# Kernel optimization log

Hardware: AMD Instinct MI355X
Metric: run time of the kernel (lower is better)

Reference implementation:

```python
import jax, jax.numpy as jnp
import numpy as np

BS, N, D = 64, 2048, 512

def setup_inputs() -> dict:
    key = jax.random.key(0)
    ks = jax.random.split(key, 9)
    M = jax.random.uniform(ks[0], (BS, N, D), dtype=jnp.float32)          # memory, uniform(0,1) like M_init
    k = jax.random.normal(ks[1], (BS, D), dtype=jnp.float32)              # key/query
    beta = 5.0 * jax.random.uniform(ks[2], (BS, 1), dtype=jnp.float32)    # content sharpness > 0
    g = jax.random.uniform(ks[3], (BS, 1), dtype=jnp.float32)             # interpolation gate in (0,1)
    s = jax.nn.softmax(jax.random.normal(ks[4], (BS, 3), dtype=jnp.float32), axis=-1)  # shift dist over [-1,0,1]
    y = 1.0 + 2.0 * jax.random.uniform(ks[5], (BS, 1), dtype=jnp.float32) # sharpen exponent >= 1
    e = jax.random.uniform(ks[6], (BS, D), dtype=jnp.float32)             # erase vector in (0,1)
    a = jax.random.normal(ks[7], (BS, D), dtype=jnp.float32)              # add vector
    w_prev = jax.nn.softmax(jax.random.normal(ks[8], (BS, N), dtype=jnp.float32), axis=-1)
    return {"M": M, "k": k, "beta": beta, "g": g, "s": s, "y": y,
            "e": e, "a": a, "w_prev": w_prev}

def reference(M, k, beta, g, s, y, e, a, w_prev):
    # --- content focus: cosine similarity, scaled by beta, softmax over N ---
    dot = jnp.einsum('bnd,bd->bn', M, k)                                   # [bs, N]
    denom = jnp.linalg.norm(M, axis=-1) * jnp.linalg.norm(k, axis=-1, keepdims=True)
    w = jax.nn.softmax((dot / denom) * beta, axis=1)
    # --- location focus: interpolate with previous weights ---
    w = g * w + (1.0 - g) * w_prev
    # --- circular convolution with 3-tap shift kernel s (offsets -1,0,+1) ---
    # original: window [w[i-1], w[i], w[i+1]] dotted with flipped s -> s2*w[i-1]+s1*w[i]+s0*w[i+1]
    w = (s[:, 2:3] * jnp.roll(w, 1, axis=1)
         + s[:, 1:2] * w
         + s[:, 0:1] * jnp.roll(w, -1, axis=1))
    # --- sharpen ---
    wp = w ** y
    w = wp / jnp.sum(wp, axis=1, keepdims=True)                            # [bs, N]
    # --- read ---
    r = jnp.einsum('bn,bnd->bd', w, M)                                     # [bs, D]
    # --- write: M[i] <- M[i] * (1 - w_i * e) + w_i * a  (diag(e) bmm == elementwise) ---
    M_next = M * (1.0 - w[:, :, None] * e[:, None, :]) + w[:, :, None] * a[:, None, :]
    return r, w, M_next
```

## Files before the change

### kernel.cpp

```cpp
#include <hip/hip_runtime.h>

#define BS 64
#define NN 2048
#define DD 512
#define ROWS 64
#define BPB (NN / ROWS)

typedef float f32x4 __attribute__((ext_vector_type(4)));

__device__ __forceinline__ float block_max(float x) {
    __shared__ float sm[4];
    int lane = threadIdx.x & 63, wid = threadIdx.x >> 6;
#pragma unroll
    for (int off = 32; off > 0; off >>= 1) x = fmaxf(x, __shfl_xor(x, off));
    if (lane == 0) sm[wid] = x;
    __syncthreads();
    x = fmaxf(fmaxf(sm[0], sm[1]), fmaxf(sm[2], sm[3]));
    __syncthreads();
    return x;
}
__device__ __forceinline__ float block_sum(float x) {
    __shared__ float sm[4];
    int lane = threadIdx.x & 63, wid = threadIdx.x >> 6;
#pragma unroll
    for (int off = 32; off > 0; off >>= 1) x += __shfl_xor(x, off);
    if (lane == 0) sm[wid] = x;
    __syncthreads();
    x = sm[0] + sm[1] + sm[2] + sm[3];
    __syncthreads();
    return x;
}

__global__ __launch_bounds__(256) void k_score(const float* __restrict__ M,
                                               const float* __restrict__ kvec,
                                               const float* __restrict__ beta,
                                               float* __restrict__ score) {
    int wave = threadIdx.x >> 6;
    int lane = threadIdx.x & 63;
    int row0 = blockIdx.x * 16 + wave * 4;
    int b    = row0 >> 11;

    const f32x4* kr = (const f32x4*)(kvec + (size_t)b * DD);
    f32x4 k0 = kr[lane], k1 = kr[lane + 64];
    float ssk = k0.x*k0.x + k0.y*k0.y + k0.z*k0.z + k0.w*k0.w
              + k1.x*k1.x + k1.y*k1.y + k1.z*k1.z + k1.w*k1.w;
#pragma unroll
    for (int off = 32; off > 0; off >>= 1) ssk += __shfl_xor(ssk, off);
    float bscale = beta[b];

    f32x4 xa[4], xb[4];
#pragma unroll
    for (int rr = 0; rr < 4; ++rr) {
        const f32x4* Mr = (const f32x4*)(M + ((size_t)row0 + rr) * DD);
        xa[rr] = Mr[lane];
        xb[rr] = Mr[lane + 64];
    }
    float dot[4], ss[4];
#pragma unroll
    for (int rr = 0; rr < 4; ++rr) {
        dot[rr] = xa[rr].x*k0.x + xa[rr].y*k0.y + xa[rr].z*k0.z + xa[rr].w*k0.w
                + xb[rr].x*k1.x + xb[rr].y*k1.y + xb[rr].z*k1.z + xb[rr].w*k1.w;
        ss[rr]  = xa[rr].x*xa[rr].x + xa[rr].y*xa[rr].y + xa[rr].z*xa[rr].z + xa[rr].w*xa[rr].w
                + xb[rr].x*xb[rr].x + xb[rr].y*xb[rr].y + xb[rr].z*xb[rr].z + xb[rr].w*xb[rr].w;
    }
#pragma unroll
    for (int off = 32; off > 0; off >>= 1) {
#pragma unroll
        for (int rr = 0; rr < 4; ++rr) {
            dot[rr] += __shfl_xor(dot[rr], off);
            ss[rr]  += __shfl_xor(ss[rr], off);
        }
    }
    if (lane == 0) {
        f32x4 sc;
        sc.x = bscale * dot[0] * rsqrtf(ss[0] * ssk);
        sc.y = bscale * dot[1] * rsqrtf(ss[1] * ssk);
        sc.z = bscale * dot[2] * rsqrtf(ss[2] * ssk);
        sc.w = bscale * dot[3] * rsqrtf(ss[3] * ssk);
        *(f32x4*)&score[row0] = sc;
    }
}

__global__ __launch_bounds__(256) void k_rw(const float* __restrict__ M,
                                            const float* __restrict__ score,
                                            const float* __restrict__ gp,
                                            const float* __restrict__ sp,
                                            const float* __restrict__ yp,
                                            const float* __restrict__ ep,
                                            const float* __restrict__ ap,
                                            const float* __restrict__ w_prev,
                                            float* __restrict__ w_out,
                                            float* __restrict__ part,
                                            float* __restrict__ Mn) {
    __shared__ float v[NN];
    __shared__ float wloc[ROWS];
    __shared__ f32x4 sacc[128];

    int blk = (int)gridDim.x - 1 - (int)blockIdx.x;
    int b   = blk / BPB;
    int q   = blk % BPB;
    int n0  = q * ROWS;
    int t   = threadIdx.x;

    float g = gp[b], y = yp[b];
    float s0 = sp[b * 3 + 0], s1 = sp[b * 3 + 1], s2 = sp[b * 3 + 2];

    float loc[8];
    float mx = -1e30f;
#pragma unroll
    for (int i = 0; i < 8; ++i) {
        loc[i] = score[(size_t)b * NN + t * 8 + i];
        mx = fmaxf(mx, loc[i]);
    }
    mx = block_max(mx);
    float sum = 0.f;
#pragma unroll
    for (int i = 0; i < 8; ++i) {
        loc[i] = __expf(loc[i] - mx);
        sum += loc[i];
    }
    sum = block_sum(sum);
    float inv = 1.f / sum;
#pragma unroll
    for (int i = 0; i < 8; ++i) {
        int n = t * 8 + i;
        v[n] = g * loc[i] * inv + (1.f - g) * w_prev[(size_t)b * NN + n];
    }
    __syncthreads();
    float u[8];
    float psum = 0.f;
#pragma unroll
    for (int i = 0; i < 8; ++i) {
        int n  = t * 8 + i;
        int nm = (n == 0) ? NN - 1 : n - 1;
        int np = (n == NN - 1) ? 0 : n + 1;
        float uu = s2 * v[nm] + s1 * v[n] + s0 * v[np];
        uu = powf(uu, y);
        u[i] = uu;
        psum += uu;
    }
    psum = block_sum(psum);
    float pin = 1.f / psum;
#pragma unroll
    for (int i = 0; i < 8; ++i) {
        int n  = t * 8 + i;
        float wf = u[i] * pin;
        if (q == 0) w_out[(size_t)b * NN + n] = wf;
        int d = n - n0;
        if (d >= 0 && d < ROWS) wloc[d] = wf;
    }
    __syncthreads();

    int c  = t & 127;
    int rh = t >> 7;
    const f32x4* e4 = (const f32x4*)(ep + (size_t)b * DD);
    const f32x4* a4 = (const f32x4*)(ap + (size_t)b * DD);
    f32x4 ev = e4[c], av = a4[c];
    f32x4 acc = (f32x4)(0.f);

    const f32x4* Mb  = (const f32x4*)(M  + ((size_t)b * NN + n0) * DD);
    f32x4*       Mnb = (f32x4*)      (Mn + ((size_t)b * NN + n0) * DD);

    float wv0[4];
    f32x4 m40[4];
#pragma unroll
    for (int j = 0; j < 4; ++j) {
        int rr = j * 2 + rh;
        wv0[j] = wloc[rr];
        m40[j] = Mb[(size_t)rr * 128 + c];
    }
#pragma unroll
    for (int i = 0; i < 8; ++i) {
        float wv1[4];
        f32x4 m41[4];
        if (i < 7) {
#pragma unroll
            for (int j = 0; j < 4; ++j) {
                int rr = ((i + 1) * 4 + j) * 2 + rh;
                wv1[j] = wloc[rr];
                m41[j] = Mb[(size_t)rr * 128 + c];
            }
        }
#pragma unroll
        for (int j = 0; j < 4; ++j) {
            int rr = (i * 4 + j) * 2 + rh;
            acc += wv0[j] * m40[j];
            f32x4 o = m40[j] * (1.f - wv0[j] * ev) + wv0[j] * av;
            __builtin_nontemporal_store(o, &Mnb[(size_t)rr * 128 + c]);
        }
#pragma unroll
        for (int j = 0; j < 4; ++j) { wv0[j] = wv1[j]; m40[j] = m41[j]; }
    }

    if (rh == 1) sacc[c] = acc;
    __syncthreads();
    if (rh == 0) {
        acc += sacc[c];
        ((f32x4*)(part + (size_t)blk * DD))[c] = acc;
    }
}

__global__ __launch_bounds__(256) void k_reduce(const float* __restrict__ part,
                                               float* __restrict__ r) {
    int b  = blockIdx.x;
    int t  = threadIdx.x;
    int c  = t & 127;
    int rh = t >> 7;
    const f32x4* pb = (const f32x4*)(part + (size_t)b * BPB * DD);
    f32x4 acc = (f32x4)(0.f);
    for (int j = rh * (BPB / 2); j < (rh + 1) * (BPB / 2); ++j) {
        acc += pb[(size_t)j * 128 + c];
    }
    __shared__ f32x4 sacc[128];
    if (rh == 1) sacc[c] = acc;
    __syncthreads();
    if (rh == 0) {
        acc += sacc[c];
        ((f32x4*)(r + (size_t)b * DD))[c] = acc;
    }
}

extern "C" void kernel_launch(void* const* d_in, const int* in_sizes, int n_in,
                              void* d_out, int out_size, void* d_ws, size_t ws_size,
                              hipStream_t stream) {
    const float* M      = (const float*)d_in[0];
    const float* k      = (const float*)d_in[1];
    const float* beta   = (const float*)d_in[2];
    const float* g      = (const float*)d_in[3];
    const float* s      = (const float*)d_in[4];
    const float* y      = (const float*)d_in[5];
    const float* e      = (const float*)d_in[6];
    const float* a      = (const float*)d_in[7];
    const float* w_prev = (const float*)d_in[8];

    float* out = (float*)d_out;
    float* r   = out;
    float* w   = out + BS * DD;
    float* Mn  = out + BS * DD + BS * NN;

    float* score = (float*)d_ws;
    float* part  = score + BS * NN;

    k_score <<<BS * NN / 16, 256, 0, stream>>>(M, k, beta, score);
    k_rw    <<<BS * BPB,     256, 0, stream>>>(M, score, g, s, y, e, a,
                                               w_prev, w, part, Mn);
    k_reduce<<<BS,           256, 0, stream>>>(part, r);
}
```

Baseline: 138.5 us.

## Fuse final read reduction into rw kernel via last-block atomic counter; double rows per block

Removes the separate reduce kernel launch. Each rw block atomically increments a per-batch counter, and the last block to finish sums the partials to produce r. Rows per block are doubled to 128, which halves the number of blocks and the redundant per-block softmax and sharpen work over the full row. The cost is fewer blocks for parallelism, plus threadfence and atomic overhead in every block.

```diff
diff --git a/kernel.cpp b/kernel.cpp
--- a/kernel.cpp
+++ b/kernel.cpp
@@ -3,7 +3,7 @@
 #define BS 64
 #define NN 2048
 #define DD 512
-#define ROWS 64
+#define ROWS 128
 #define BPB (NN / ROWS)
 
 typedef float f32x4 __attribute__((ext_vector_type(4)));
@@ -34,7 +34,10 @@
 __global__ __launch_bounds__(256) void k_score(const float* __restrict__ M,
                                                const float* __restrict__ kvec,
                                                const float* __restrict__ beta,
-                                               float* __restrict__ score) {
+                                               float* __restrict__ score,
+                                               int* __restrict__ cnt) {
+    if (blockIdx.x == 0 && threadIdx.x < BS) cnt[threadIdx.x] = 0;
+
     int wave = threadIdx.x >> 6;
     int lane = threadIdx.x & 63;
     int row0 = blockIdx.x * 16 + wave * 4;
@@ -91,10 +94,13 @@
                                             const float* __restrict__ w_prev,
                                             float* __restrict__ w_out,
                                             float* __restrict__ part,
+                                            int* __restrict__ cnt,
+                                            float* __restrict__ r,
                                             float* __restrict__ Mn) {
     __shared__ float v[NN];
     __shared__ float wloc[ROWS];
     __shared__ f32x4 sacc[128];
+    __shared__ int isLast;
 
     int blk = (int)gridDim.x - 1 - (int)blockIdx.x;
     int b   = blk / BPB;
@@ -170,10 +176,10 @@
         m40[j] = Mb[(size_t)rr * 128 + c];
     }
 #pragma unroll
-    for (int i = 0; i < 8; ++i) {
+    for (int i = 0; i < ROWS / 8; ++i) {
         float wv1[4];
         f32x4 m41[4];
-        if (i < 7) {
+        if (i < ROWS / 8 - 1) {
 #pragma unroll
             for (int j = 0; j < 4; ++j) {
                 int rr = ((i + 1) * 4 + j) * 2 + rh;
@@ -198,25 +204,28 @@
         acc += sacc[c];
         ((f32x4*)(part + (size_t)blk * DD))[c] = acc;
     }
-}
-
-__global__ __launch_bounds__(256) void k_reduce(const float* __restrict__ part,
-                                               float* __restrict__ r) {
-    int b  = blockIdx.x;
-    int t  = threadIdx.x;
-    int c  = t & 127;
-    int rh = t >> 7;
-    const f32x4* pb = (const f32x4*)(part + (size_t)b * BPB * DD);
-    f32x4 acc = (f32x4)(0.f);
-    for (int j = rh * (BPB / 2); j < (rh + 1) * (BPB / 2); ++j) {
-        acc += pb[(size_t)j * 128 + c];
-    }
-    __shared__ f32x4 sacc[128];
-    if (rh == 1) sacc[c] = acc;
-    __syncthreads();
-    if (rh == 0) {
-        acc += sacc[c];
-        ((f32x4*)(r + (size_t)b * DD))[c] = acc;
+    __syncthreads();
+
+    if (t == 0) {
+        __threadfence();
+        int old = atomicAdd(&cnt[b], 1);
+        isLast = (old == BPB - 1);
+    }
+    __syncthreads();
+    if (isLast) {
+        if (t == 0) __threadfence();
+        __syncthreads();
+        const f32x4* pb = (const f32x4*)(part + (size_t)b * BPB * DD);
+        f32x4 racc = (f32x4)(0.f);
+        for (int j = rh * (BPB / 2); j < (rh + 1) * (BPB / 2); ++j) {
+            racc += pb[(size_t)j * 128 + c];
+        }
+        if (rh == 1) sacc[c] = racc;
+        __syncthreads();
+        if (rh == 0) {
+            racc += sacc[c];
+            ((f32x4*)(r + (size_t)b * DD))[c] = racc;
+        }
     }
 }
 
@@ -240,9 +249,9 @@
 
     float* score = (float*)d_ws;
     float* part  = score + BS * NN;
-
-    k_score <<<BS * NN / 16, 256, 0, stream>>>(M, k, beta, score);
-    k_rw    <<<BS * BPB,     256, 0, stream>>>(M, score, g, s, y, e, a,
-                                               w_prev, w, part, Mn);
-    k_reduce<<<BS,           256, 0, stream>>>(part, r);
-}
+    int*   cnt   = (int*)(part + BS * BPB * DD);
+
+    k_score<<<BS * NN / 16, 256, 0, stream>>>(M, k, beta, score, cnt);
+    k_rw   <<<BS * BPB,     256, 0, stream>>>(M, score, g, s, y, e, a,
+                                              w_prev, w, part, cnt, r, Mn);
+}
```

Result: slower. 195.4 us (+41.1%).
